# Performance work log

Hardware: AMD Instinct MI355X
Metric: run time of the kernel (lower is better)

## Reference

```python
import jax, jax.numpy as jnp
import numpy as np

STATE_DIM = 64
NUM_CHANNELS = 128
BATCH = 8
SEQ_LEN = 4096
DT = 0.01


def hippo_matrix(n):
    # hippo[i,j] = sqrt(2i+1)*sqrt(2j+1) if i>j, (i+1) if i==j, 0 otherwise; A = -hippo
    i = np.arange(n)[:, None]
    j = np.arange(n)[None, :]
    m = np.where(i > j, np.sqrt(2 * i + 1.0) * np.sqrt(2 * j + 1.0), 0.0)
    m = m + np.diag(np.arange(1, n + 1).astype(np.float64))
    return jnp.asarray(-m, dtype=jnp.float32)


def setup_inputs() -> dict:
    key = jax.random.key(0)
    k1, k2, k3 = jax.random.split(key, 3)
    signal = jax.random.normal(k1, (BATCH, NUM_CHANNELS, SEQ_LEN), dtype=jnp.float32)
    B = jax.random.normal(k2, (STATE_DIM, NUM_CHANNELS), dtype=jnp.float32) * 0.1
    C = jax.random.normal(k3, (STATE_DIM, NUM_CHANNELS), dtype=jnp.float32) * 0.1
    A = hippo_matrix(STATE_DIM)
    return {"signal": signal, "B": B, "C": C, "A": A, "dt": DT}


def reference(signal, B, C, A, dt):
    n = A.shape[0]
    eye = jnp.eye(n, dtype=signal.dtype)
    # Bilinear (Tustin) discretization, same as the torch module
    inv = jnp.linalg.inv(eye - dt * 0.5 * A)
    A_bar = inv @ (eye + dt * 0.5 * A)          # [N, N]
    B_bar = dt * (inv @ B)                       # [N, C]

    def step(state, x_t):
        # state: [b, n, c], x_t: [b, c]
        state = jnp.einsum('nm,bmc->bnc', A_bar, state) + B_bar[None] * x_t[:, None, :]
        y = jnp.einsum('nc,bnc->bc', C, state)   # sum over state dim
        return state, y

    x = jnp.moveaxis(signal, -1, 0)              # [L, b, c]
    state0 = jnp.zeros((signal.shape[0], n, signal.shape[1]), dtype=signal.dtype)
    _, ys = jax.lax.scan(step, state0, x)        # ys: [L, b, c]
    return jnp.moveaxis(ys, 0, -1)               # [b, c, L]
```

## Files before the change

### kernel.cpp

```cpp
#include <hip/hip_runtime.h>

#define N 64
#define NC 128
#define NB 8
#define LSEQ 4096
#define QC 128
#define NCHUNK 32

#define OFF_ABAR 0
#define OFF_AQ   4096
#define OFF_BBAR 8192
#define OFF_ABT  16384
#define OFF_A2   20480
#define OFF_A2T  24576
#define OFF_A4   28672
#define OFF_A4T  32768
#define OFF_FS   36864
#define U16_BASE (OFF_FS + NCHUNK*NB*NC*N)

#define OFF_WH 0
#define OFF_WL (OFF_WH + NC*N*QC)
#define OFF_UH (OFF_WL + NC*N*QC)
#define OFF_UL (OFF_UH + NC*QC*N)
#define OFF_KH (OFF_UL + NC*QC*N)
#define OFF_KL (OFF_KH + NC*256)
#define OFF_SH (OFF_KL + NC*256)
#define OFF_SL (OFF_SH + NCHUNK*NB*NC*N)

typedef __attribute__((ext_vector_type(8)))  __bf16 bf16x8;
typedef __attribute__((ext_vector_type(16))) float  f32x16;
typedef __attribute__((ext_vector_type(4)))  unsigned int u32x4;

__device__ __forceinline__ float rdlane(float v, int l) {
    return __int_as_float(__builtin_amdgcn_readlane(__float_as_int(v), l));
}

__device__ __forceinline__ void load_row64(const float* __restrict__ p, float (&ar)[64]) {
    const float4* rp = reinterpret_cast<const float4*>(p);
#pragma unroll
    for (int t = 0; t < 16; ++t) {
        float4 v = rp[t];
        ar[4*t+0] = v.x; ar[4*t+1] = v.y; ar[4*t+2] = v.z; ar[4*t+3] = v.w;
    }
}

__device__ __forceinline__ float matvec64(const float (&ar)[64], float v) {
    float a0 = 0.f, a1 = 0.f, a2 = 0.f, a3 = 0.f;
#pragma unroll
    for (int m = 0; m < 64; m += 4) {
        a0 += ar[m+0] * rdlane(v, m+0);
        a1 += ar[m+1] * rdlane(v, m+1);
        a2 += ar[m+2] * rdlane(v, m+2);
        a3 += ar[m+3] * rdlane(v, m+3);
    }
    return (a0 + a1) + (a2 + a3);
}

__device__ __forceinline__ void f2bf_hl(float x, unsigned short& hi, unsigned short& lo) {
    unsigned u = __float_as_uint(x);
    unsigned r = (u + 0x7fffu + ((u >> 16) & 1u)) >> 16;
    hi = (unsigned short)r;
    float fh = __uint_as_float(r << 16);
    float l  = x - fh;
    unsigned ul = __float_as_uint(l);
    unsigned rl = (ul + 0x7fffu + ((ul >> 16) & 1u)) >> 16;
    lo = (unsigned short)rl;
}

__device__ __forceinline__ unsigned pack_hl2(float x0, float x1, unsigned& lo32) {
    unsigned short h0, l0, h1, l1;
    f2bf_hl(x0, h0, l0); f2bf_hl(x1, h1, l1);
    lo32 = (unsigned)l0 | ((unsigned)l1 << 16);
    return (unsigned)h0 | ((unsigned)h1 << 16);
}

__device__ __forceinline__ bf16x8 ld_frag(const unsigned short* p) {
    u32x4 v = *(const u32x4*)p;
    return __builtin_bit_cast(bf16x8, v);
}

__device__ __forceinline__ bf16x8 pack8(const unsigned short* v) {
    u32x4 u;
    u.x = v[0] | ((unsigned)v[1] << 16);
    u.y = v[2] | ((unsigned)v[3] << 16);
    u.z = v[4] | ((unsigned)v[5] << 16);
    u.w = v[6] | ((unsigned)v[7] << 16);
    return __builtin_bit_cast(bf16x8, u);
}

__global__ __launch_bounds__(256) void prep_cols_kernel(const float* __restrict__ A,
    const float* __restrict__ B, const float* __restrict__ dtp,
    float* __restrict__ ws)
{
    __shared__ float AT[64*65];
    const int tid  = threadIdx.x;
    const int wave = tid >> 6;
    const int l    = tid & 63;
    const float dt = dtp[0];
    const float h  = 0.5f * dt;

    for (int idx = tid; idx < 64*64; idx += 256) {
        int row = idx >> 6, i = idx & 63;
        AT[i*65 + row] = A[idx];
    }
    __syncthreads();

    const float rdv = 1.0f / (1.0f - h * AT[l*65 + l]);
    const int colid = blockIdx.x * 4 + wave;

    float r;
    if (colid < 64) {
        int j = colid;
        r = ((l == j) ? 1.0f : 0.0f) + h * AT[j*65 + l];
    } else {
        int c = colid - 64;
        r = B[l*NC + c];
    }

#pragma unroll
    for (int i = 0; i < 64; ++i) {
        float xi = rdlane(r, i) * rdlane(rdv, i);
        float a  = AT[i*65 + l];
        r = fmaf(h * xi, a, r);
        r = (l == i) ? xi : r;
    }

    if (colid < 64) {
        ws[OFF_ABAR + l*64 + colid] = r;
        ws[OFF_ABT  + colid*64 + l] = r;
    } else {
        ws[OFF_BBAR + l*NC + (colid - 64)] = dt * r;
    }
}

__global__ __launch_bounds__(256) void pow_sq_kernel(const float* __restrict__ src,
    const float* __restrict__ srcT, float* __restrict__ dst, float* __restrict__ dstT)
{
    const int tid = threadIdx.x;
    const int wave = tid >> 6;
    const int l = tid & 63;
    const int j = blockIdx.x * 4 + wave;

    float ar[64];
    load_row64(src + l*64, ar);
    float x = srcT[j*64 + l];
    float y = matvec64(ar, x);
    dst[l*64 + j]  = y;
    dstT[j*64 + l] = y;
}

__global__ __launch_bounds__(256, 1) void chains_kernel(const float* __restrict__ C,
    float* __restrict__ ws)
{
    __shared__ float Wlds[128][65];
    __shared__ float karr[128];
    __shared__ float seed[3][64];
    unsigned short* u16b = (unsigned short*)(ws + U16_BASE);
    const int bid = blockIdx.x;
    const int tid = threadIdx.x;
    const int w4  = tid >> 6;
    const int l   = tid & 63;

    if (bid < 128) {
        const int c = bid;
        float a4[64];
        load_row64(ws + OFF_A4 + l*64, a4);
        const float Cl = C[l*NC + c];
        float cur;
        if (w4 == 0) {
            float ab[64];
            load_row64(ws + OFF_ABAR + l*64, ab);
            float t = ws[OFF_BBAR + l*NC + c];
            cur = t;
            t = matvec64(ab, t); seed[0][l] = t;
            t = matvec64(ab, t); seed[1][l] = t;
            t = matvec64(ab, t); seed[2][l] = t;
        }
        __syncthreads();
        if (w4 > 0) cur = seed[w4 - 1][l];
        int p = w4;
#pragma unroll 1
        for (int it = 0; it < 32; ++it) {
            Wlds[p][l] = cur;
            float d = Cl * cur;
            d += __shfl_xor(d, 32, 64); d += __shfl_xor(d, 16, 64);
            d += __shfl_xor(d, 8, 64);  d += __shfl_xor(d, 4, 64);
            d += __shfl_xor(d, 2, 64);  d += __shfl_xor(d, 1, 64);
            if (l == 0) karr[p] = d;
            if (it < 31) { cur = matvec64(a4, cur); p += 4; }
        }
        __syncthreads();
        for (int idx = tid; idx < 64*64; idx += 256) {
            int n = idx >> 6, i2 = idx & 63;
            int kq = i2*2;
            float w0 = Wlds[127 - kq][n];
            float w1 = Wlds[126 - kq][n];
            unsigned lo32, hi32 = pack_hl2(w0, w1, lo32);
            ((unsigned*)(u16b + OFF_WH + (c*64 + n)*128))[i2] = hi32;
            ((unsigned*)(u16b + OFF_WL + (c*64 + n)*128))[i2] = lo32;
        }
        if (tid < 128) {
            int i = tid;
            float k0 = (2*i   < 128) ? karr[127 - 2*i] : 0.0f;
            float k1 = (2*i+1 < 128) ? karr[126 - 2*i] : 0.0f;
            unsigned lo32, hi32 = pack_hl2(k0, k1, lo32);
            ((unsigned*)(u16b + OFF_KH + c*256))[i] = hi32;
            ((unsigned*)(u16b + OFF_KL + c*256))[i] = lo32;
        }
    } else if (bid < 256) {
        const int c = bid - 128;
        float a4t[64];
        load_row64(ws + OFF_A4T + l*64, a4t);
        float cur;
        if (w4 == 0) {
            float abt[64];
            load_row64(ws + OFF_ABT + l*64, abt);
            float t = C[l*NC + c];
            t = matvec64(abt, t); cur = t;
            t = matvec64(abt, t); seed[0][l] = t;
            t = matvec64(abt, t); seed[1][l] = t;
            t = matvec64(abt, t); seed[2][l] = t;
        }
        __syncthreads();
        if (w4 > 0) cur = seed[w4 - 1][l];
        int q = w4;
#pragma unroll 1
        for (int it = 0; it < 32; ++it) {
            unsigned short hi, lo; f2bf_hl(cur, hi, lo);
            u16b[OFF_UH + (c*QC + q)*64 + l] = hi;
            u16b[OFF_UL + (c*QC + q)*64 + l] = lo;
            if (it < 31) { cur = matvec64(a4t, cur); q += 4; }
        }
    } else {
        const int j = (bid - 256)*4 + w4;
        float a4[64];
        load_row64(ws + OFF_A4 + l*64, a4);
        float cur = (l == j) ? 1.0f : 0.0f;
#pragma unroll 1
        for (int it = 0; it < 32; ++it) cur = matvec64(a4, cur);
        ws[OFF_AQ + l*64 + j] = cur;
    }
}

__global__ __launch_bounds__(256, 2) void fchunk_mfma_kernel(const float* __restrict__ x,
    float* __restrict__ ws)
{
    __shared__ __align__(16) unsigned Xh32[64*68], Xl32[64*68];
    const unsigned short* u16b = (const unsigned short*)(ws + U16_BASE);
    const int tid = threadIdx.x;
    const int c = blockIdx.x;
    const int g = blockIdx.y;

    for (int idx = tid; idx < 64*64; idx += 256) {
        int col = idx >> 6, i2 = idx & 63;
        int j = g*8 + (col >> 3), b = col & 7;
        const float2 xv = *reinterpret_cast<const float2*>(
            x + ((long)(b*NC + c))*LSEQ + j*QC + i2*2);
        unsigned lo32, hi32 = pack_hl2(xv.x, xv.y, lo32);
        Xh32[col*68 + i2] = hi32;
        Xl32[col*68 + i2] = lo32;
    }
    __syncthreads();

    const int l = tid & 63;
    const int w = tid >> 6;
    const int lane2 = l & 31;
    const int h = l >> 5;
    const int mt = w & 1;
    const int nt = w >> 1;

    const unsigned short* Xh = (const unsigned short*)Xh32;
    const unsigned short* Xl = (const unsigned short*)Xl32;
    const unsigned short* WHp = u16b + OFF_WH + (c*64 + mt*32 + lane2)*128 + 8*h;
    const unsigned short* WLp = u16b + OFF_WL + (c*64 + mt*32 + lane2)*128 + 8*h;

    f32x16 a0 = {}, a1 = {}, a2 = {};
#pragma unroll
    for (int t = 0; t < 8; ++t) {
        bf16x8 ah = ld_frag(WHp + 16*t);
        bf16x8 al = ld_frag(WLp + 16*t);
        bf16x8 bh = ld_frag(&Xh[(nt*32 + lane2)*136 + 16*t + 8*h]);
        bf16x8 bl = ld_frag(&Xl[(nt*32 + lane2)*136 + 16*t + 8*h]);
        a0 = __builtin_amdgcn_mfma_f32_32x32x16_bf16(ah, bh, a0, 0, 0, 0);
        a1 = __builtin_amdgcn_mfma_f32_32x32x16_bf16(al, bh, a1, 0, 0, 0);
        a2 = __builtin_amdgcn_mfma_f32_32x32x16_bf16(ah, bl, a2, 0, 0, 0);
    }
    f32x16 s = a0 + a1 + a2;
    const int col = g*64 + nt*32 + lane2;
    const int j = col >> 3, b = col & 7;
#pragma unroll
    for (int r = 0; r < 16; ++r) {
        int n = mt*32 + (r & 3) + 8*(r >> 2) + 4*h;
        ws[OFF_FS + ((j*NB + b)*NC + c)*N + n] = s[r];
    }
}

__global__ __launch_bounds__(64) void scan_kernel(float* __restrict__ ws)
{
    unsigned short* u16b = (unsigned short*)(ws + U16_BASE);
    const int l = threadIdx.x;
    const int b = blockIdx.x >> 7;
    const int c = blockIdx.x & 127;

    float aq[64];
    load_row64(ws + OFF_AQ + l*64, aq);

    u16b[OFF_SH + ((0*NB + b)*NC + c)*64 + l] = 0;
    u16b[OFF_SL + ((0*NB + b)*NC + c)*64 + l] = 0;

    float s = ws[OFF_FS + ((0*NB + b)*NC + c)*N + l];
    {
        unsigned short hi, lo; f2bf_hl(s, hi, lo);
        u16b[OFF_SH + ((1*NB + b)*NC + c)*64 + l] = hi;
        u16b[OFF_SL + ((1*NB + b)*NC + c)*64 + l] = lo;
    }
    for (int j = 1; j <= NCHUNK - 2; ++j) {
        float f = ws[OFF_FS + ((j*NB + b)*NC + c)*N + l];
        float a0 = f, a1 = 0.f, a2 = 0.f, a3 = 0.f;
#pragma unroll
        for (int m = 0; m < 64; m += 4) {
            a0 += aq[m+0] * rdlane(s, m+0);
            a1 += aq[m+1] * rdlane(s, m+1);
            a2 += aq[m+2] * rdlane(s, m+2);
            a3 += aq[m+3] * rdlane(s, m+3);
        }
        s = (a0 + a1) + (a2 + a3);
        unsigned short hi, lo; f2bf_hl(s, hi, lo);
        u16b[OFF_SH + (((j+1)*NB + b)*NC + c)*64 + l] = hi;
        u16b[OFF_SL + (((j+1)*NB + b)*NC + c)*64 + l] = lo;
    }
}

__global__ __launch_bounds__(256, 2) void output_mfma_kernel(const float* __restrict__ x,
    const float* __restrict__ ws, float* __restrict__ out)
{
    __shared__ __align__(16) unsigned krh32[128], krl32[128];
    __shared__ __align__(16) unsigned Xh32[64*68], Xl32[64*68];
    const unsigned short* u16b = (const unsigned short*)(ws + U16_BASE);
    const int tid = threadIdx.x;
    const int c = blockIdx.x;
    const int g = blockIdx.y;

    if (tid < 128) {
        krh32[tid] = ((const unsigned*)(u16b + OFF_KH + c*256))[tid];
        krl32[tid] = ((const unsigned*)(u16b + OFF_KL + c*256))[tid];
    }
    for (int idx = tid; idx < 64*64; idx += 256) {
        int col = idx >> 6, i2 = idx & 63;
        int j = g*8 + (col >> 3), b = col & 7;
        const float2 xv = *reinterpret_cast<const float2*>(
            x + ((long)(b*NC + c))*LSEQ + j*QC + i2*2);
        unsigned lo32, hi32 = pack_hl2(xv.x, xv.y, lo32);
        Xh32[col*68 + i2] = hi32;
        Xl32[col*68 + i2] = lo32;
    }
    __syncthreads();

    const int l = tid & 63;
    const int w = tid >> 6;
    const int lane2 = l & 31;
    const int h = l >> 5;
    const int m = w*32 + lane2;

    const unsigned short* krh = (const unsigned short*)krh32;
    const unsigned short* krl = (const unsigned short*)krl32;
    const unsigned short* Xh = (const unsigned short*)Xh32;
    const unsigned short* Xl = (const unsigned short*)Xl32;

    f32x16 a0[2] = {{}, {}}, a1[2] = {{}, {}}, a2[2] = {{}, {}};

#pragma unroll
    for (int t = 0; t < 12; ++t) {
        bf16x8 ah, al;
        if (t < 8) {
            int I0 = 127 - m + 16*t + 8*h;
            unsigned short vh[8], vl[8];
#pragma unroll
            for (int e = 0; e < 8; ++e) { vh[e] = krh[I0 + e]; vl[e] = krl[I0 + e]; }
            ah = pack8(vh); al = pack8(vl);
        } else {
            const unsigned short* up = u16b + (c*QC + m)*64 + 16*(t-8) + 8*h;
            ah = ld_frag(up + OFF_UH);
            al = ld_frag(up + OFF_UL);
        }
#pragma unroll
        for (int nt = 0; nt < 2; ++nt) {
            bf16x8 bh, bl;
            if (t < 8) {
                bh = ld_frag(&Xh[(nt*32 + lane2)*136 + 16*t + 8*h]);
                bl = ld_frag(&Xl[(nt*32 + lane2)*136 + 16*t + 8*h]);
            } else {
                int col = g*64 + nt*32 + lane2;
                int j = col >> 3, b = col & 7;
                const unsigned short* sp = u16b + ((j*NB + b)*NC + c)*64 + 16*(t-8) + 8*h;
                bh = ld_frag(sp + OFF_SH);
                bl = ld_frag(sp + OFF_SL);
            }
            a0[nt] = __builtin_amdgcn_mfma_f32_32x32x16_bf16(ah, bh, a0[nt], 0, 0, 0);
            a1[nt] = __builtin_amdgcn_mfma_f32_32x32x16_bf16(al, bh, a1[nt], 0, 0, 0);
            a2[nt] = __builtin_amdgcn_mfma_f32_32x32x16_bf16(ah, bl, a2[nt], 0, 0, 0);
        }
    }

#pragma unroll
    for (int nt = 0; nt < 2; ++nt) {
        f32x16 s = a0[nt] + a1[nt] + a2[nt];
        int col = g*64 + nt*32 + lane2;
        int j = col >> 3, b = col & 7;
        float* op = out + ((long)(b*NC + c))*LSEQ + j*QC;
#pragma unroll
        for (int r = 0; r < 16; ++r) {
            int row = w*32 + (r & 3) + 8*(r >> 2) + 4*h;
            op[row] = s[r];
        }
    }
}

extern "C" void kernel_launch(void* const* d_in, const int* in_sizes, int n_in,
                              void* d_out, int out_size, void* d_ws, size_t ws_size,
                              hipStream_t stream)
{
    const float* signal = (const float*)d_in[0];
    const float* B      = (const float*)d_in[1];
    const float* C      = (const float*)d_in[2];
    const float* A      = (const float*)d_in[3];
    const float* dt     = (const float*)d_in[4];
    float* ws  = (float*)d_ws;
    float* out = (float*)d_out;

    hipLaunchKernelGGL(prep_cols_kernel,  dim3(48),     dim3(256), 0, stream, A, B, dt, ws);
    hipLaunchKernelGGL(pow_sq_kernel,     dim3(16),     dim3(256), 0, stream,
                       ws + OFF_ABAR, ws + OFF_ABT, ws + OFF_A2, ws + OFF_A2T);
    hipLaunchKernelGGL(pow_sq_kernel,     dim3(16),     dim3(256), 0, stream,
                       ws + OFF_A2, ws + OFF_A2T, ws + OFF_A4, ws + OFF_A4T);
    hipLaunchKernelGGL(chains_kernel,     dim3(272),    dim3(256), 0, stream, C, ws);
    hipLaunchKernelGGL(fchunk_mfma_kernel,dim3(NC, 4),  dim3(256), 0, stream, signal, ws);
    hipLaunchKernelGGL(scan_kernel,       dim3(NB*NC),  dim3(64),  0, stream, ws);
    hipLaunchKernelGGL(output_mfma_kernel,dim3(NC, 4),  dim3(256), 0, stream, signal, ws, out);
}
```

Measured before the change: 83.10 us.

## Fuse setup kernels and merge chunk-forcing, scan and intra-chunk output per channel

Discretization, B_bar and the A^2/A^4 squarings are merged into one single-block setup kernel that keeps intermediates in LDS. B_bar is now computed as h*(A_bar*B + B), which reuses the A_bar matrix. The per-chunk forcing MFMA, the intra-chunk convolution output and the inter-chunk scan are fused into one kernel per channel with 512 threads, and the forcing terms stay in LDS instead of going through global memory. The state-contribution term is split into a separate kernel that does a read-modify-write on the output. Launch count and global traffic drop, but the fused kernel runs only 128 blocks and serializes its four groups, which reduces parallelism.

```diff
diff --git a/kernel.cpp b/kernel.cpp
--- a/kernel.cpp
+++ b/kernel.cpp
@@ -11,10 +11,8 @@
 #define OFF_AQ   4096
 #define OFF_BBAR 8192
 #define OFF_ABT  16384
-#define OFF_A2   20480
-#define OFF_A2T  24576
-#define OFF_A4   28672
-#define OFF_A4T  32768
+#define OFF_A4   20480
+#define OFF_A4T  24576
 #define OFF_FS   36864
 #define U16_BASE (OFF_FS + NCHUNK*NB*NC*N)
 
@@ -88,65 +86,78 @@
     return __builtin_bit_cast(bf16x8, u);
 }
 
-__global__ __launch_bounds__(256) void prep_cols_kernel(const float* __restrict__ A,
-    const float* __restrict__ B, const float* __restrict__ dtp,
-    float* __restrict__ ws)
+__global__ __launch_bounds__(1024) void setup_kernel(const float* __restrict__ A,
+    const float* __restrict__ B, const float* __restrict__ dtp, float* __restrict__ ws)
 {
     __shared__ float AT[64*65];
-    const int tid  = threadIdx.x;
-    const int wave = tid >> 6;
-    const int l    = tid & 63;
+    __shared__ float Ab[64*65];
+    __shared__ float AbT[64*65];
+    __shared__ float A2T[64*65];
+    const int tid = threadIdx.x;
+    const int wv  = tid >> 6;
+    const int l   = tid & 63;
     const float dt = dtp[0];
     const float h  = 0.5f * dt;
 
-    for (int idx = tid; idx < 64*64; idx += 256) {
+    for (int idx = tid; idx < 4096; idx += 1024) {
         int row = idx >> 6, i = idx & 63;
         AT[i*65 + row] = A[idx];
     }
     __syncthreads();
-
     const float rdv = 1.0f / (1.0f - h * AT[l*65 + l]);
-    const int colid = blockIdx.x * 4 + wave;
-
-    float r;
-    if (colid < 64) {
-        int j = colid;
-        r = ((l == j) ? 1.0f : 0.0f) + h * AT[j*65 + l];
-    } else {
-        int c = colid - 64;
-        r = B[l*NC + c];
-    }
-
-#pragma unroll
-    for (int i = 0; i < 64; ++i) {
-        float xi = rdlane(r, i) * rdlane(rdv, i);
-        float a  = AT[i*65 + l];
-        r = fmaf(h * xi, a, r);
-        r = (l == i) ? xi : r;
-    }
-
-    if (colid < 64) {
-        ws[OFF_ABAR + l*64 + colid] = r;
-        ws[OFF_ABT  + colid*64 + l] = r;
-    } else {
-        ws[OFF_BBAR + l*NC + (colid - 64)] = dt * r;
-    }
-}
-
-__global__ __launch_bounds__(256) void pow_sq_kernel(const float* __restrict__ src,
-    const float* __restrict__ srcT, float* __restrict__ dst, float* __restrict__ dstT)
-{
-    const int tid = threadIdx.x;
-    const int wave = tid >> 6;
-    const int l = tid & 63;
-    const int j = blockIdx.x * 4 + wave;
-
+
+#pragma unroll 1
+    for (int rep = 0; rep < 4; ++rep) {
+        const int j = wv + rep*16;
+        float r = ((l == j) ? 1.0f : 0.0f) + h * AT[j*65 + l];
+#pragma unroll
+        for (int i = 0; i < 64; ++i) {
+            float xi = rdlane(r, i) * rdlane(rdv, i);
+            r = fmaf(h * xi, AT[i*65 + l], r);
+            r = (l == i) ? xi : r;
+        }
+        Ab[l*65 + j]  = r;
+        AbT[j*65 + l] = r;
+    }
+    __syncthreads();
+
+    for (int idx = tid; idx < 4096; idx += 1024) {
+        int i = idx >> 6, j = idx & 63;
+        ws[OFF_ABAR + idx] = Ab[i*65 + j];
+        ws[OFF_ABT + idx]  = AbT[i*65 + j];
+    }
     float ar[64];
-    load_row64(src + l*64, ar);
-    float x = srcT[j*64 + l];
-    float y = matvec64(ar, x);
-    dst[l*64 + j]  = y;
-    dstT[j*64 + l] = y;
+#pragma unroll
+    for (int m2 = 0; m2 < 64; ++m2) ar[m2] = Ab[l*65 + m2];
+
+#pragma unroll 1
+    for (int rep = 0; rep < 4; ++rep) {
+        const int j = wv + rep*16;
+        float v = AbT[j*65 + l];
+        float y = matvec64(ar, v);
+        AT[l*65 + j]  = y;
+        A2T[j*65 + l] = y;
+    }
+#pragma unroll 1
+    for (int rep = 0; rep < 8; ++rep) {
+        const int c = wv + rep*16;
+        float v = B[l*NC + c];
+        float y = matvec64(ar, v);
+        ws[OFF_BBAR + l*NC + c] = h * (y + v);
+    }
+    __syncthreads();
+
+    float a2r[64];
+#pragma unroll
+    for (int m2 = 0; m2 < 64; ++m2) a2r[m2] = AT[l*65 + m2];
+#pragma unroll 1
+    for (int rep = 0; rep < 4; ++rep) {
+        const int j = wv + rep*16;
+        float v = A2T[j*65 + l];
+        float y = matvec64(a2r, v);
+        ws[OFF_A4 + l*64 + j]  = y;
+        ws[OFF_A4T + j*64 + l] = y;
+    }
 }
 
 __global__ __launch_bounds__(256, 1) void chains_kernel(const float* __restrict__ C,
@@ -242,176 +253,174 @@
     }
 }
 
-__global__ __launch_bounds__(256, 2) void fchunk_mfma_kernel(const float* __restrict__ x,
-    float* __restrict__ ws)
+__global__ __launch_bounds__(512) void fused_kernel(const float* __restrict__ x,
+    float* __restrict__ ws, float* __restrict__ out)
 {
+    __shared__ float F_lds[NCHUNK*NB*64];
     __shared__ __align__(16) unsigned Xh32[64*68], Xl32[64*68];
-    const unsigned short* u16b = (const unsigned short*)(ws + U16_BASE);
+    __shared__ __align__(16) unsigned krh32[128], krl32[128];
+    unsigned short* u16b = (unsigned short*)(ws + U16_BASE);
     const int tid = threadIdx.x;
     const int c = blockIdx.x;
-    const int g = blockIdx.y;
-
-    for (int idx = tid; idx < 64*64; idx += 256) {
-        int col = idx >> 6, i2 = idx & 63;
-        int j = g*8 + (col >> 3), b = col & 7;
-        const float2 xv = *reinterpret_cast<const float2*>(
-            x + ((long)(b*NC + c))*LSEQ + j*QC + i2*2);
-        unsigned lo32, hi32 = pack_hl2(xv.x, xv.y, lo32);
-        Xh32[col*68 + i2] = hi32;
-        Xl32[col*68 + i2] = lo32;
-    }
-    __syncthreads();
-
+    const int w = tid >> 6;
     const int l = tid & 63;
-    const int w = tid >> 6;
     const int lane2 = l & 31;
     const int h = l >> 5;
-    const int mt = w & 1;
-    const int nt = w >> 1;
-
-    const unsigned short* Xh = (const unsigned short*)Xh32;
-    const unsigned short* Xl = (const unsigned short*)Xl32;
-    const unsigned short* WHp = u16b + OFF_WH + (c*64 + mt*32 + lane2)*128 + 8*h;
-    const unsigned short* WLp = u16b + OFF_WL + (c*64 + mt*32 + lane2)*128 + 8*h;
-
-    f32x16 a0 = {}, a1 = {}, a2 = {};
-#pragma unroll
-    for (int t = 0; t < 8; ++t) {
-        bf16x8 ah = ld_frag(WHp + 16*t);
-        bf16x8 al = ld_frag(WLp + 16*t);
-        bf16x8 bh = ld_frag(&Xh[(nt*32 + lane2)*136 + 16*t + 8*h]);
-        bf16x8 bl = ld_frag(&Xl[(nt*32 + lane2)*136 + 16*t + 8*h]);
-        a0 = __builtin_amdgcn_mfma_f32_32x32x16_bf16(ah, bh, a0, 0, 0, 0);
-        a1 = __builtin_amdgcn_mfma_f32_32x32x16_bf16(al, bh, a1, 0, 0, 0);
-        a2 = __builtin_amdgcn_mfma_f32_32x32x16_bf16(ah, bl, a2, 0, 0, 0);
-    }
-    f32x16 s = a0 + a1 + a2;
-    const int col = g*64 + nt*32 + lane2;
-    const int j = col >> 3, b = col & 7;
-#pragma unroll
-    for (int r = 0; r < 16; ++r) {
-        int n = mt*32 + (r & 3) + 8*(r >> 2) + 4*h;
-        ws[OFF_FS + ((j*NB + b)*NC + c)*N + n] = s[r];
-    }
-}
-
-__global__ __launch_bounds__(64) void scan_kernel(float* __restrict__ ws)
-{
-    unsigned short* u16b = (unsigned short*)(ws + U16_BASE);
-    const int l = threadIdx.x;
-    const int b = blockIdx.x >> 7;
-    const int c = blockIdx.x & 127;
-
-    float aq[64];
-    load_row64(ws + OFF_AQ + l*64, aq);
-
-    u16b[OFF_SH + ((0*NB + b)*NC + c)*64 + l] = 0;
-    u16b[OFF_SL + ((0*NB + b)*NC + c)*64 + l] = 0;
-
-    float s = ws[OFF_FS + ((0*NB + b)*NC + c)*N + l];
-    {
-        unsigned short hi, lo; f2bf_hl(s, hi, lo);
-        u16b[OFF_SH + ((1*NB + b)*NC + c)*64 + l] = hi;
-        u16b[OFF_SL + ((1*NB + b)*NC + c)*64 + l] = lo;
-    }
-    for (int j = 1; j <= NCHUNK - 2; ++j) {
-        float f = ws[OFF_FS + ((j*NB + b)*NC + c)*N + l];
-        float a0 = f, a1 = 0.f, a2 = 0.f, a3 = 0.f;
-#pragma unroll
-        for (int m = 0; m < 64; m += 4) {
-            a0 += aq[m+0] * rdlane(s, m+0);
-            a1 += aq[m+1] * rdlane(s, m+1);
-            a2 += aq[m+2] * rdlane(s, m+2);
-            a3 += aq[m+3] * rdlane(s, m+3);
-        }
-        s = (a0 + a1) + (a2 + a3);
-        unsigned short hi, lo; f2bf_hl(s, hi, lo);
-        u16b[OFF_SH + (((j+1)*NB + b)*NC + c)*64 + l] = hi;
-        u16b[OFF_SL + (((j+1)*NB + b)*NC + c)*64 + l] = lo;
-    }
-}
-
-__global__ __launch_bounds__(256, 2) void output_mfma_kernel(const float* __restrict__ x,
-    const float* __restrict__ ws, float* __restrict__ out)
-{
-    __shared__ __align__(16) unsigned krh32[128], krl32[128];
-    __shared__ __align__(16) unsigned Xh32[64*68], Xl32[64*68];
-    const unsigned short* u16b = (const unsigned short*)(ws + U16_BASE);
-    const int tid = threadIdx.x;
-    const int c = blockIdx.x;
-    const int g = blockIdx.y;
 
     if (tid < 128) {
         krh32[tid] = ((const unsigned*)(u16b + OFF_KH + c*256))[tid];
         krl32[tid] = ((const unsigned*)(u16b + OFF_KL + c*256))[tid];
     }
-    for (int idx = tid; idx < 64*64; idx += 256) {
-        int col = idx >> 6, i2 = idx & 63;
-        int j = g*8 + (col >> 3), b = col & 7;
-        const float2 xv = *reinterpret_cast<const float2*>(
-            x + ((long)(b*NC + c))*LSEQ + j*QC + i2*2);
-        unsigned lo32, hi32 = pack_hl2(xv.x, xv.y, lo32);
-        Xh32[col*68 + i2] = hi32;
-        Xl32[col*68 + i2] = lo32;
+    const unsigned short* Xh = (const unsigned short*)Xh32;
+    const unsigned short* Xl = (const unsigned short*)Xl32;
+    const unsigned short* krh = (const unsigned short*)krh32;
+    const unsigned short* krl = (const unsigned short*)krl32;
+
+#pragma unroll 1
+    for (int g = 0; g < 4; ++g) {
+        __syncthreads();
+        for (int idx = tid; idx < 64*64; idx += 512) {
+            int col = idx >> 6, i2 = idx & 63;
+            int j = g*8 + (col >> 3), b = col & 7;
+            const float2 xv = *reinterpret_cast<const float2*>(
+                x + ((long)(b*NC + c))*LSEQ + j*QC + i2*2);
+            unsigned lo32, hi32 = pack_hl2(xv.x, xv.y, lo32);
+            Xh32[col*68 + i2] = hi32;
+            Xl32[col*68 + i2] = lo32;
+        }
+        __syncthreads();
+
+        if (w < 4) {
+            const int mt = w & 1, ntf = w >> 1;
+            const unsigned short* WHp = u16b + OFF_WH + (c*64 + mt*32 + lane2)*128 + 8*h;
+            const unsigned short* WLp = u16b + OFF_WL + (c*64 + mt*32 + lane2)*128 + 8*h;
+            f32x16 f0 = {}, f1 = {}, f2 = {};
+#pragma unroll
+            for (int t = 0; t < 8; ++t) {
+                bf16x8 ah = ld_frag(WHp + 16*t);
+                bf16x8 al = ld_frag(WLp + 16*t);
+                bf16x8 bh = ld_frag(&Xh[(ntf*32 + lane2)*136 + 16*t + 8*h]);
+                bf16x8 bl = ld_frag(&Xl[(ntf*32 + lane2)*136 + 16*t + 8*h]);
+                f0 = __builtin_amdgcn_mfma_f32_32x32x16_bf16(ah, bh, f0, 0, 0, 0);
+                f1 = __builtin_amdgcn_mfma_f32_32x32x16_bf16(al, bh, f1, 0, 0, 0);
+                f2 = __builtin_amdgcn_mfma_f32_32x32x16_bf16(ah, bl, f2, 0, 0, 0);
+            }
+            f32x16 s = f0 + f1 + f2;
+            const int col = ntf*32 + lane2;
+            const int j = g*8 + (col >> 3), b = col & 7;
+#pragma unroll
+            for (int r = 0; r < 16; ++r) {
+                int n = mt*32 + (r & 3) + 8*(r >> 2) + 4*h;
+                F_lds[(j*NB + b)*64 + n] = s[r];
+            }
+        } else {
+            const int m = (w - 4)*32 + lane2;
+            f32x16 a0[2] = {{}, {}}, a1[2] = {{}, {}}, a2[2] = {{}, {}};
+#pragma unroll
+            for (int t = 0; t < 8; ++t) {
+                int I0 = 127 - m + 16*t + 8*h;
+                unsigned short vh[8], vl[8];
+#pragma unroll
+                for (int e = 0; e < 8; ++e) { vh[e] = krh[I0 + e]; vl[e] = krl[I0 + e]; }
+                bf16x8 ah = pack8(vh), al = pack8(vl);
+#pragma unroll
+                for (int nt = 0; nt < 2; ++nt) {
+                    bf16x8 bh = ld_frag(&Xh[(nt*32 + lane2)*136 + 16*t + 8*h]);
+                    bf16x8 bl = ld_frag(&Xl[(nt*32 + lane2)*136 + 16*t + 8*h]);
+                    a0[nt] = __builtin_amdgcn_mfma_f32_32x32x16_bf16(ah, bh, a0[nt], 0, 0, 0);
+                    a1[nt] = __builtin_amdgcn_mfma_f32_32x32x16_bf16(al, bh, a1[nt], 0, 0, 0);
+                    a2[nt] = __builtin_amdgcn_mfma_f32_32x32x16_bf16(ah, bl, a2[nt], 0, 0, 0);
+                }
+            }
+#pragma unroll
+            for (int nt = 0; nt < 2; ++nt) {
+                f32x16 s = a0[nt] + a1[nt] + a2[nt];
+                int col = g*64 + nt*32 + lane2;
+                int j = col >> 3, b = col & 7;
+                float* op = out + ((long)(b*NC + c))*LSEQ + j*QC;
+#pragma unroll
+                for (int r = 0; r < 16; ++r) {
+                    int row = (w - 4)*32 + (r & 3) + 8*(r >> 2) + 4*h;
+                    op[row] = s[r];
+                }
+            }
+        }
     }
     __syncthreads();
 
+    {
+        const int b = w;
+        float aq[64];
+        load_row64(ws + OFF_AQ + l*64, aq);
+
+        u16b[OFF_SH + ((0*NB + b)*NC + c)*64 + l] = 0;
+        u16b[OFF_SL + ((0*NB + b)*NC + c)*64 + l] = 0;
+        float s = F_lds[(0*NB + b)*64 + l];
+        {
+            unsigned short hi, lo; f2bf_hl(s, hi, lo);
+            u16b[OFF_SH + ((1*NB + b)*NC + c)*64 + l] = hi;
+            u16b[OFF_SL + ((1*NB + b)*NC + c)*64 + l] = lo;
+        }
+#pragma unroll 1
+        for (int j2 = 1; j2 <= NCHUNK - 2; ++j2) {
+            float f = F_lds[(j2*NB + b)*64 + l];
+            float a0 = f, a1 = 0.f, a2 = 0.f, a3 = 0.f;
+#pragma unroll
+            for (int m2 = 0; m2 < 64; m2 += 4) {
+                a0 += aq[m2+0] * rdlane(s, m2+0);
+                a1 += aq[m2+1] * rdlane(s, m2+1);
+                a2 += aq[m2+2] * rdlane(s, m2+2);
+                a3 += aq[m2+3] * rdlane(s, m2+3);
+            }
+            s = (a0 + a1) + (a2 + a3);
+            unsigned short hi, lo; f2bf_hl(s, hi, lo);
+            u16b[OFF_SH + (((j2+1)*NB + b)*NC + c)*64 + l] = hi;
+            u16b[OFF_SL + (((j2+1)*NB + b)*NC + c)*64 + l] = lo;
+        }
+    }
+}
+
+__global__ __launch_bounds__(256, 4) void usadd_kernel(const float* __restrict__ ws,
+    float* __restrict__ out)
+{
+    const unsigned short* u16b = (const unsigned short*)(ws + U16_BASE);
+    const int tid = threadIdx.x;
+    const int c = blockIdx.x >> 2;
+    const int g = blockIdx.x & 3;
     const int l = tid & 63;
     const int w = tid >> 6;
     const int lane2 = l & 31;
     const int h = l >> 5;
     const int m = w*32 + lane2;
 
-    const unsigned short* krh = (const unsigned short*)krh32;
-    const unsigned short* krl = (const unsigned short*)krl32;
-    const unsigned short* Xh = (const unsigned short*)Xh32;
-    const unsigned short* Xl = (const unsigned short*)Xl32;
-
-    f32x16 a0[2] = {{}, {}}, a1[2] = {{}, {}}, a2[2] = {{}, {}};
-
-#pragma unroll
-    for (int t = 0; t < 12; ++t) {
-        bf16x8 ah, al;
-        if (t < 8) {
-            int I0 = 127 - m + 16*t + 8*h;
-            unsigned short vh[8], vl[8];
-#pragma unroll
-            for (int e = 0; e < 8; ++e) { vh[e] = krh[I0 + e]; vl[e] = krl[I0 + e]; }
-            ah = pack8(vh); al = pack8(vl);
-        } else {
-            const unsigned short* up = u16b + (c*QC + m)*64 + 16*(t-8) + 8*h;
-            ah = ld_frag(up + OFF_UH);
-            al = ld_frag(up + OFF_UL);
-        }
+    f32x16 c0[2] = {{}, {}}, c1[2] = {{}, {}}, c2[2] = {{}, {}};
+#pragma unroll
+    for (int t = 0; t < 4; ++t) {
+        const unsigned short* up = u16b + (c*QC + m)*64 + 16*t + 8*h;
+        bf16x8 ah = ld_frag(up + OFF_UH);
+        bf16x8 al = ld_frag(up + OFF_UL);
 #pragma unroll
         for (int nt = 0; nt < 2; ++nt) {
-            bf16x8 bh, bl;
-            if (t < 8) {
-                bh = ld_frag(&Xh[(nt*32 + lane2)*136 + 16*t + 8*h]);
-                bl = ld_frag(&Xl[(nt*32 + lane2)*136 + 16*t + 8*h]);
-            } else {
-                int col = g*64 + nt*32 + lane2;
-                int j = col >> 3, b = col & 7;
-                const unsigned short* sp = u16b + ((j*NB + b)*NC + c)*64 + 16*(t-8) + 8*h;
-                bh = ld_frag(sp + OFF_SH);
-                bl = ld_frag(sp + OFF_SL);
-            }
-            a0[nt] = __builtin_amdgcn_mfma_f32_32x32x16_bf16(ah, bh, a0[nt], 0, 0, 0);
-            a1[nt] = __builtin_amdgcn_mfma_f32_32x32x16_bf16(al, bh, a1[nt], 0, 0, 0);
-            a2[nt] = __builtin_amdgcn_mfma_f32_32x32x16_bf16(ah, bl, a2[nt], 0, 0, 0);
-        }
-    }
-
+            int col = g*64 + nt*32 + lane2;
+            int j = col >> 3, b = col & 7;
+            const unsigned short* sp = u16b + ((j*NB + b)*NC + c)*64 + 16*t + 8*h;
+            bf16x8 bh = ld_frag(sp + OFF_SH);
+            bf16x8 bl = ld_frag(sp + OFF_SL);
+            c0[nt] = __builtin_amdgcn_mfma_f32_32x32x16_bf16(ah, bh, c0[nt], 0, 0, 0);
+            c1[nt] = __builtin_amdgcn_mfma_f32_32x32x16_bf16(al, bh, c1[nt], 0, 0, 0);
+            c2[nt] = __builtin_amdgcn_mfma_f32_32x32x16_bf16(ah, bl, c2[nt], 0, 0, 0);
+        }
+    }
 #pragma unroll
     for (int nt = 0; nt < 2; ++nt) {
-        f32x16 s = a0[nt] + a1[nt] + a2[nt];
+        f32x16 s = (c0[nt] + c1[nt]) + c2[nt];
         int col = g*64 + nt*32 + lane2;
         int j = col >> 3, b = col & 7;
         float* op = out + ((long)(b*NC + c))*LSEQ + j*QC;
 #pragma unroll
         for (int r = 0; r < 16; ++r) {
             int row = w*32 + (r & 3) + 8*(r >> 2) + 4*h;
-            op[row] = s[r];
+            op[row] += s[r];
         }
     }
 }
@@ -428,13 +437,8 @@
     float* ws  = (float*)d_ws;
     float* out = (float*)d_out;
 
-    hipLaunchKernelGGL(prep_cols_kernel,  dim3(48),     dim3(256), 0, stream, A, B, dt, ws);
-    hipLaunchKernelGGL(pow_sq_kernel,     dim3(16),     dim3(256), 0, stream,
-                       ws + OFF_ABAR, ws + OFF_ABT, ws + OFF_A2, ws + OFF_A2T);
-    hipLaunchKernelGGL(pow_sq_kernel,     dim3(16),     dim3(256), 0, stream,
-                       ws + OFF_A2, ws + OFF_A2T, ws + OFF_A4, ws + OFF_A4T);
-    hipLaunchKernelGGL(chains_kernel,     dim3(272),    dim3(256), 0, stream, C, ws);
-    hipLaunchKernelGGL(fchunk_mfma_kernel,dim3(NC, 4),  dim3(256), 0, stream, signal, ws);
-    hipLaunchKernelGGL(scan_kernel,       dim3(NB*NC),  dim3(64),  0, stream, ws);
-    hipLaunchKernelGGL(output_mfma_kernel,dim3(NC, 4),  dim3(256), 0, stream, signal, ws, out);
-}
+    hipLaunchKernelGGL(setup_kernel,  dim3(1),    dim3(1024), 0, stream, A, B, dt, ws);
+    hipLaunchKernelGGL(chains_kernel, dim3(272),  dim3(256),  0, stream, C, ws);
+    hipLaunchKernelGGL(fused_kernel,  dim3(NC),   dim3(512),  0, stream, signal, ws, out);
+    hipLaunchKernelGGL(usadd_kernel,  dim3(NC*4), dim3(256),  0, stream, ws, out);
+}
```

Measured after the change: 127.9 us. 53.9% more time.

## Fuse discretization and matrix squaring into one setup kernel; precompute Toeplitz tiles

Applied to the files above, without the earlier changes.

Merges the prep and two squaring kernels into a single 1024-thread block that computes A_bar, B_bar (derived as h*(A_bar*B + B)) and A^4 through shared memory, removing two kernel launches and their global round trips. The chains kernel now materializes the full lower-triangular Toeplitz matrix of the C·A^k kernel in bf16 hi/lo form per channel, so the output MFMA kernel loads A fragments with vector loads instead of gathering scalars from LDS. The cost is a serial single-block setup phase and a much larger workspace write/read for the Toeplitz tiles.

```diff
diff --git a/kernel.cpp b/kernel.cpp
--- a/kernel.cpp
+++ b/kernel.cpp
@@ -11,10 +11,8 @@
 #define OFF_AQ   4096
 #define OFF_BBAR 8192
 #define OFF_ABT  16384
-#define OFF_A2   20480
-#define OFF_A2T  24576
-#define OFF_A4   28672
-#define OFF_A4T  32768
+#define OFF_A4   20480
+#define OFF_A4T  24576
 #define OFF_FS   36864
 #define U16_BASE (OFF_FS + NCHUNK*NB*NC*N)
 
@@ -22,9 +20,9 @@
 #define OFF_WL (OFF_WH + NC*N*QC)
 #define OFF_UH (OFF_WL + NC*N*QC)
 #define OFF_UL (OFF_UH + NC*QC*N)
-#define OFF_KH (OFF_UL + NC*QC*N)
-#define OFF_KL (OFF_KH + NC*256)
-#define OFF_SH (OFF_KL + NC*256)
+#define OFF_TH (OFF_UL + NC*QC*N)
+#define OFF_TL (OFF_TH + NC*QC*QC)
+#define OFF_SH (OFF_TL + NC*QC*QC)
 #define OFF_SL (OFF_SH + NCHUNK*NB*NC*N)
 
 typedef __attribute__((ext_vector_type(8)))  __bf16 bf16x8;
@@ -79,74 +77,78 @@
     return __builtin_bit_cast(bf16x8, v);
 }
 
-__device__ __forceinline__ bf16x8 pack8(const unsigned short* v) {
-    u32x4 u;
-    u.x = v[0] | ((unsigned)v[1] << 16);
-    u.y = v[2] | ((unsigned)v[3] << 16);
-    u.z = v[4] | ((unsigned)v[5] << 16);
-    u.w = v[6] | ((unsigned)v[7] << 16);
-    return __builtin_bit_cast(bf16x8, u);
-}
-
-__global__ __launch_bounds__(256) void prep_cols_kernel(const float* __restrict__ A,
-    const float* __restrict__ B, const float* __restrict__ dtp,
-    float* __restrict__ ws)
+__global__ __launch_bounds__(1024) void setup_kernel(const float* __restrict__ A,
+    const float* __restrict__ B, const float* __restrict__ dtp, float* __restrict__ ws)
 {
     __shared__ float AT[64*65];
-    const int tid  = threadIdx.x;
-    const int wave = tid >> 6;
-    const int l    = tid & 63;
+    __shared__ float Ab[64*65];
+    __shared__ float AbT[64*65];
+    __shared__ float A2T[64*65];
+    const int tid = threadIdx.x;
+    const int wv  = tid >> 6;
+    const int l   = tid & 63;
     const float dt = dtp[0];
     const float h  = 0.5f * dt;
 
-    for (int idx = tid; idx < 64*64; idx += 256) {
+    for (int idx = tid; idx < 4096; idx += 1024) {
         int row = idx >> 6, i = idx & 63;
         AT[i*65 + row] = A[idx];
     }
     __syncthreads();
-
     const float rdv = 1.0f / (1.0f - h * AT[l*65 + l]);
-    const int colid = blockIdx.x * 4 + wave;
-
-    float r;
-    if (colid < 64) {
-        int j = colid;
-        r = ((l == j) ? 1.0f : 0.0f) + h * AT[j*65 + l];
-    } else {
-        int c = colid - 64;
-        r = B[l*NC + c];
-    }
-
-#pragma unroll
-    for (int i = 0; i < 64; ++i) {
-        float xi = rdlane(r, i) * rdlane(rdv, i);
-        float a  = AT[i*65 + l];
-        r = fmaf(h * xi, a, r);
-        r = (l == i) ? xi : r;
-    }
-
-    if (colid < 64) {
-        ws[OFF_ABAR + l*64 + colid] = r;
-        ws[OFF_ABT  + colid*64 + l] = r;
-    } else {
-        ws[OFF_BBAR + l*NC + (colid - 64)] = dt * r;
-    }
-}
-
-__global__ __launch_bounds__(256) void pow_sq_kernel(const float* __restrict__ src,
-    const float* __restrict__ srcT, float* __restrict__ dst, float* __restrict__ dstT)
-{
-    const int tid = threadIdx.x;
-    const int wave = tid >> 6;
-    const int l = tid & 63;
-    const int j = blockIdx.x * 4 + wave;
-
+
+#pragma unroll 1
+    for (int rep = 0; rep < 4; ++rep) {
+        const int j = wv + rep*16;
+        float r = ((l == j) ? 1.0f : 0.0f) + h * AT[j*65 + l];
+#pragma unroll
+        for (int i = 0; i < 64; ++i) {
+            float xi = rdlane(r, i) * rdlane(rdv, i);
+            r = fmaf(h * xi, AT[i*65 + l], r);
+            r = (l == i) ? xi : r;
+        }
+        Ab[l*65 + j]  = r;
+        AbT[j*65 + l] = r;
+    }
+    __syncthreads();
+
+    for (int idx = tid; idx < 4096; idx += 1024) {
+        int i = idx >> 6, j = idx & 63;
+        ws[OFF_ABAR + idx] = Ab[i*65 + j];
+        ws[OFF_ABT + idx]  = AbT[i*65 + j];
+    }
     float ar[64];
-    load_row64(src + l*64, ar);
-    float x = srcT[j*64 + l];
-    float y = matvec64(ar, x);
-    dst[l*64 + j]  = y;
-    dstT[j*64 + l] = y;
+#pragma unroll
+    for (int m2 = 0; m2 < 64; ++m2) ar[m2] = Ab[l*65 + m2];
+
+#pragma unroll 1
+    for (int rep = 0; rep < 4; ++rep) {
+        const int j = wv + rep*16;
+        float v = AbT[j*65 + l];
+        float y = matvec64(ar, v);
+        AT[l*65 + j]  = y;
+        A2T[j*65 + l] = y;
+    }
+#pragma unroll 1
+    for (int rep = 0; rep < 8; ++rep) {
+        const int c = wv + rep*16;
+        float v = B[l*NC + c];
+        float y = matvec64(ar, v);
+        ws[OFF_BBAR + l*NC + c] = h * (y + v);
+    }
+    __syncthreads();
+
+    float a2r[64];
+#pragma unroll
+    for (int m2 = 0; m2 < 64; ++m2) a2r[m2] = AT[l*65 + m2];
+#pragma unroll 1
+    for (int rep = 0; rep < 4; ++rep) {
+        const int j = wv + rep*16;
+        float v = A2T[j*65 + l];
+        float y = matvec64(a2r, v);
+        ws[OFF_A4 + l*64 + j]  = y;
+        ws[OFF_A4T + j*64 + l] = y;
+    }
 }
 
 __global__ __launch_bounds__(256, 1) void chains_kernel(const float* __restrict__ C,
@@ -199,13 +201,14 @@
             ((unsigned*)(u16b + OFF_WH + (c*64 + n)*128))[i2] = hi32;
             ((unsigned*)(u16b + OFF_WL + (c*64 + n)*128))[i2] = lo32;
         }
-        if (tid < 128) {
-            int i = tid;
-            float k0 = (2*i   < 128) ? karr[127 - 2*i] : 0.0f;
-            float k1 = (2*i+1 < 128) ? karr[126 - 2*i] : 0.0f;
-            unsigned lo32, hi32 = pack_hl2(k0, k1, lo32);
-            ((unsigned*)(u16b + OFF_KH + c*256))[i] = hi32;
-            ((unsigned*)(u16b + OFF_KL + c*256))[i] = lo32;
+        for (int idx = tid; idx < 128*64; idx += 256) {
+            int q = idx >> 6, i2 = idx & 63;
+            int kk = i2*2;
+            float t0 = (kk     <= q) ? karr[q - kk]     : 0.0f;
+            float t1 = (kk + 1 <= q) ? karr[q - kk - 1] : 0.0f;
+            unsigned lo32, hi32 = pack_hl2(t0, t1, lo32);
+            ((unsigned*)(u16b + OFF_TH + (c*QC + q)*QC))[i2] = hi32;
+            ((unsigned*)(u16b + OFF_TL + (c*QC + q)*QC))[i2] = lo32;
         }
     } else if (bid < 256) {
         const int c = bid - 128;
@@ -334,17 +337,12 @@
 __global__ __launch_bounds__(256, 2) void output_mfma_kernel(const float* __restrict__ x,
     const float* __restrict__ ws, float* __restrict__ out)
 {
-    __shared__ __align__(16) unsigned krh32[128], krl32[128];
     __shared__ __align__(16) unsigned Xh32[64*68], Xl32[64*68];
     const unsigned short* u16b = (const unsigned short*)(ws + U16_BASE);
     const int tid = threadIdx.x;
     const int c = blockIdx.x;
     const int g = blockIdx.y;
 
-    if (tid < 128) {
-        krh32[tid] = ((const unsigned*)(u16b + OFF_KH + c*256))[tid];
-        krl32[tid] = ((const unsigned*)(u16b + OFF_KL + c*256))[tid];
-    }
     for (int idx = tid; idx < 64*64; idx += 256) {
         int col = idx >> 6, i2 = idx & 63;
         int j = g*8 + (col >> 3), b = col & 7;
@@ -362,10 +360,10 @@
     const int h = l >> 5;
     const int m = w*32 + lane2;
 
-    const unsigned short* krh = (const unsigned short*)krh32;
-    const unsigned short* krl = (const unsigned short*)krl32;
     const unsigned short* Xh = (const unsigned short*)Xh32;
     const unsigned short* Xl = (const unsigned short*)Xl32;
+    const unsigned short* THp = u16b + OFF_TH + (c*QC + m)*QC + 8*h;
+    const unsigned short* TLp = u16b + OFF_TL + (c*QC + m)*QC + 8*h;
 
     f32x16 a0[2] = {{}, {}}, a1[2] = {{}, {}}, a2[2] = {{}, {}};
 
@@ -373,11 +371,8 @@
     for (int t = 0; t < 12; ++t) {
         bf16x8 ah, al;
         if (t < 8) {
-            int I0 = 127 - m + 16*t + 8*h;
-            unsigned short vh[8], vl[8];
-#pragma unroll
-            for (int e = 0; e < 8; ++e) { vh[e] = krh[I0 + e]; vl[e] = krl[I0 + e]; }
-            ah = pack8(vh); al = pack8(vl);
+            ah = ld_frag(THp + 16*t);
+            al = ld_frag(TLp + 16*t);
         } else {
             const unsigned short* up = u16b + (c*QC + m)*64 + 16*(t-8) + 8*h;
             ah = ld_frag(up + OFF_UH);
@@ -428,13 +423,9 @@
     float* ws  = (float*)d_ws;
     float* out = (float*)d_out;
 
-    hipLaunchKernelGGL(prep_cols_kernel,  dim3(48),     dim3(256), 0, stream, A, B, dt, ws);
-    hipLaunchKernelGGL(pow_sq_kernel,     dim3(16),     dim3(256), 0, stream,
-                       ws + OFF_ABAR, ws + OFF_ABT, ws + OFF_A2, ws + OFF_A2T);
-    hipLaunchKernelGGL(pow_sq_kernel,     dim3(16),     dim3(256), 0, stream,
-                       ws + OFF_A2, ws + OFF_A2T, ws + OFF_A4, ws + OFF_A4T);
-    hipLaunchKernelGGL(chains_kernel,     dim3(272),    dim3(256), 0, stream, C, ws);
-    hipLaunchKernelGGL(fchunk_mfma_kernel,dim3(NC, 4),  dim3(256), 0, stream, signal, ws);
-    hipLaunchKernelGGL(scan_kernel,       dim3(NB*NC),  dim3(64),  0, stream, ws);
-    hipLaunchKernelGGL(output_mfma_kernel,dim3(NC, 4),  dim3(256), 0, stream, signal, ws, out);
-}
+    hipLaunchKernelGGL(setup_kernel,      dim3(1),     dim3(1024), 0, stream, A, B, dt, ws);
+    hipLaunchKernelGGL(chains_kernel,     dim3(272),   dim3(256),  0, stream, C, ws);
+    hipLaunchKernelGGL(fchunk_mfma_kernel,dim3(NC, 4), dim3(256),  0, stream, signal, ws);
+    hipLaunchKernelGGL(scan_kernel,       dim3(NB*NC), dim3(64),   0, stream, ws);
+    hipLaunchKernelGGL(output_mfma_kernel,dim3(NC, 4), dim3(256),  0, stream, signal, ws, out);
+}
```

After: 109.3 us. +31.5%, slower.
